# Optimization experiments

Measured on AMD Instinct MI355X. Metric: run time of the kernel, lower is better.

Reference implementation:

```python
import jax, jax.numpy as jnp
import numpy as np

N, IN_DIM, OUT_DIM, HEADS = 50000, 256, 256, 8
C = OUT_DIM // HEADS  # per-head channels = 32
E = 800000
G = 64  # number of graphs in the batch
NEG_SLOPE = 0.2
GN_EPS = 1e-5


def setup_inputs() -> dict:
    key = jax.random.key(0)
    ks = jax.random.split(key, 12)
    x = jax.random.normal(ks[0], (N, IN_DIM), dtype=jnp.float32)
    edge_index = jax.random.randint(ks[1], (2, E), 0, N, dtype=jnp.int64)
    batch = jnp.sort(jax.random.randint(ks[2], (N,), 0, G, dtype=jnp.int64))
    s = 1.0 / np.sqrt(IN_DIM)
    W_l = jax.random.uniform(ks[3], (IN_DIM, HEADS * C), jnp.float32, -s, s)
    b_l = jnp.zeros((HEADS * C,), jnp.float32)
    W_r = jax.random.uniform(ks[4], (IN_DIM, HEADS * C), jnp.float32, -s, s)
    b_r = jnp.zeros((HEADS * C,), jnp.float32)
    att = jax.random.normal(ks[5], (HEADS, C), dtype=jnp.float32) / np.sqrt(C)
    bias = jnp.zeros((HEADS * C,), jnp.float32)
    gn_weight = jnp.ones((OUT_DIM,), jnp.float32)
    gn_bias = jnp.zeros((OUT_DIM,), jnp.float32)
    gn_mean_scale = jnp.ones((OUT_DIM,), jnp.float32)
    return {"x": x, "edge_index": edge_index, "batch": batch,
            "W_l": W_l, "b_l": b_l, "W_r": W_r, "b_r": b_r,
            "att": att, "bias": bias, "gn_weight": gn_weight,
            "gn_bias": gn_bias, "gn_mean_scale": gn_mean_scale}


def _gat_block(x, src, dst, batch, W_l, b_l, W_r, b_r, att, bias,
               gn_weight, gn_bias, gn_mean_scale):
    n = x.shape[0]
    # GATv2Conv (add_self_loops=True, concat=True)
    loops = jnp.arange(n, dtype=src.dtype)
    src = jnp.concatenate([src, loops])
    dst = jnp.concatenate([dst, loops])
    xl = (x @ W_l + b_l).reshape(n, HEADS, C)  # source transform
    xr = (x @ W_r + b_r).reshape(n, HEADS, C)  # target transform
    e = jax.nn.leaky_relu(xl[src] + xr[dst], NEG_SLOPE)  # [E', H, C]
    logits = jnp.einsum('ehc,hc->eh', e, att)            # [E', H]
    # segment softmax over incoming edges of each destination node
    m = jax.ops.segment_max(logits, dst, num_segments=n)
    alpha = jnp.exp(logits - m[dst])
    denom = jax.ops.segment_sum(alpha, dst, num_segments=n)
    alpha = alpha / (denom[dst] + 1e-16)
    msg = xl[src] * alpha[:, :, None]                    # [E', H, C]
    h = jax.ops.segment_sum(msg, dst, num_segments=n).reshape(n, HEADS * C) + bias
    # identity residual (in_dim == out_dim) + ELU
    h = jax.nn.elu(h + x)
    # GraphNorm (post-norm)
    counts = jnp.maximum(jax.ops.segment_sum(jnp.ones((n,), h.dtype), batch,
                                             num_segments=G), 1.0)
    mean = jax.ops.segment_sum(h, batch, num_segments=G) / counts[:, None]
    out0 = h - gn_mean_scale * mean[batch]
    var = jax.ops.segment_sum(out0 * out0, batch, num_segments=G) / counts[:, None]
    return gn_weight * out0 / jnp.sqrt(var[batch] + GN_EPS) + gn_bias


def reference(x, edge_index, batch, W_l, b_l, W_r, b_r, att, bias,
              gn_weight, gn_bias, gn_mean_scale):
    return _gat_block(x, edge_index[0], edge_index[1], batch,
                      W_l, b_l, W_r, b_r, att, bias,
                      gn_weight, gn_bias, gn_mean_scale)
```

## Files before the change

### kernel.cpp

```cpp
#include <hip/hip_runtime.h>
#include <hip/hip_bf16.h>
#include <stdint.h>

#define N_NODES 50000
#define MPAD    50048
#define IN_DIM  256
#define EDGES   800000
#define EPRIME  (EDGES + N_NODES)
#define NGRAPH  64
#define GN_EPS  1e-5f
#define ECPAD   53248
#define SEG     52
#define SEG4    13

typedef __attribute__((ext_vector_type(8))) short short8;
typedef __attribute__((ext_vector_type(4))) float floatx4;
typedef __attribute__((ext_vector_type(2))) float float2v;

__device__ __forceinline__ unsigned short f2b(float f) {
    uint32_t u = __float_as_uint(f);
    u += 0x7fffu + ((u >> 16) & 1u);
    return (unsigned short)(u >> 16);
}
__device__ __forceinline__ float b2f(unsigned short u) {
    return __uint_as_float(((uint32_t)u) << 16);
}

__global__ __launch_bounds__(256) void k_prep_w(const float* __restrict__ Wl,
                                                const float* __restrict__ Wr,
                                                unsigned short* __restrict__ Wt) {
    int idx = blockIdx.x * 256 + threadIdx.x;
    int n = idx >> 8, k = idx & 255;
    float v = (n < 256) ? Wl[k * 256 + n] : Wr[k * 256 + (n - 256)];
    Wt[idx] = f2b(v);
}

__global__ __launch_bounds__(512) void k_gemm(const float* __restrict__ x,
                                              const unsigned short* __restrict__ Wt,
                                              const float* __restrict__ bl,
                                              const float* __restrict__ br,
                                              unsigned short* __restrict__ XL,
                                              unsigned short* __restrict__ XR) {
    __shared__ unsigned short As[64 * 256];
    int rbase = blockIdx.x * 64;
    int tid = threadIdx.x;

#pragma unroll
    for (int it = 0; it < 4; ++it) {
        int c = it * 512 + tid;
        int row = c >> 5, ch = c & 31;
        int gr = rbase + row;
        float4 f0, f1;
        if (gr < N_NODES) {
            const float4* src = (const float4*)(x + (size_t)gr * 256 + ch * 8);
            f0 = src[0]; f1 = src[1];
        } else {
            f0 = make_float4(0.f,0.f,0.f,0.f); f1 = f0;
        }
        short8 hv;
        hv[0] = (short)f2b(f0.x); hv[1] = (short)f2b(f0.y);
        hv[2] = (short)f2b(f0.z); hv[3] = (short)f2b(f0.w);
        hv[4] = (short)f2b(f1.x); hv[5] = (short)f2b(f1.y);
        hv[6] = (short)f2b(f1.z); hv[7] = (short)f2b(f1.w);
        *(short8*)(As + row * 256 + (ch ^ (row & 7)) * 8) = hv;
    }
    __syncthreads();

    int w = tid >> 6;
    int l = tid & 63;
    int m = l & 15, q = l >> 4;

    floatx4 acc[4][4];
#pragma unroll
    for (int rf = 0; rf < 4; ++rf)
#pragma unroll
        for (int cf = 0; cf < 4; ++cf)
            acc[rf][cf] = (floatx4){0.f, 0.f, 0.f, 0.f};

    const unsigned short* wbase = Wt + (size_t)(w * 64) * 256;

#pragma unroll
    for (int kk = 0; kk < 8; ++kk) {
        short8 a[4];
#pragma unroll
        for (int rf = 0; rf < 4; ++rf) {
            int row = rf * 16 + m;
            int ch = (kk * 4 + q) ^ (row & 7);
            a[rf] = *(const short8*)(As + row * 256 + ch * 8);
        }
#pragma unroll
        for (int cf = 0; cf < 4; ++cf) {
            short8 b = *(const short8*)(wbase + (size_t)(cf * 16 + m) * 256 + kk * 32 + q * 8);
#pragma unroll
            for (int rf = 0; rf < 4; ++rf)
                acc[rf][cf] = __builtin_amdgcn_mfma_f32_16x16x32_bf16(b, a[rf], acc[rf][cf], 0, 0, 0);
        }
    }

    unsigned short* obase = (w < 4) ? XL : XR;
    const float* bptr = (w < 4) ? bl : br;
    int cb = (w & 3) * 64;
#pragma unroll
    for (int cf = 0; cf < 4; ++cf) {
        int chb = cb + cf * 16 + q * 4;
        float4 bv = *(const float4*)(bptr + chb);
#pragma unroll
        for (int rf = 0; rf < 4; ++rf) {
            int node = rbase + rf * 16 + m;
            ushort4 o;
            o.x = f2b(acc[rf][cf][0] + bv.x);
            o.y = f2b(acc[rf][cf][1] + bv.y);
            o.z = f2b(acc[rf][cf][2] + bv.z);
            o.w = f2b(acc[rf][cf][3] + bv.w);
            *(ushort4*)(obase + (size_t)node * 256 + chb) = o;
        }
    }
}

__global__ __launch_bounds__(256) void k_hist(const int* __restrict__ ei,
                                              const int* __restrict__ batch,
                                              int* __restrict__ ecount,
                                              int* __restrict__ ncount) {
    __shared__ int hist[NGRAPH];
    if (threadIdx.x < NGRAPH) hist[threadIdx.x] = 0;
    __syncthreads();
    int e = blockIdx.x * 256 + threadIdx.x;
    if (e < EPRIME) {
        int d = (e < EDGES) ? ei[EDGES + e] : (e - EDGES);
        atomicAdd(&ecount[d], 1);
    }
    if (e < N_NODES) atomicAdd(&hist[batch[e]], 1);
    __syncthreads();
    if (threadIdx.x < NGRAPH && hist[threadIdx.x])
        atomicAdd(&ncount[threadIdx.x], hist[threadIdx.x]);
}

__global__ __launch_bounds__(1024) void k_scan(const int* __restrict__ ecount,
                                               int* __restrict__ estart,
                                               int* __restrict__ ecursor) {
    __shared__ int buf[1024];
    int t = threadIdx.x;
    int base = t * SEG;
    int4 v[SEG4];
    int sum = 0;
#pragma unroll
    for (int j = 0; j < SEG4; ++j) {
        v[j] = ((const int4*)(ecount + base))[j];
        sum += v[j].x + v[j].y + v[j].z + v[j].w;
    }
    buf[t] = sum;
    __syncthreads();
    for (int off = 1; off < 1024; off <<= 1) {
        int p = (t >= off) ? buf[t - off] : 0;
        __syncthreads();
        buf[t] += p;
        __syncthreads();
    }
    int run = buf[t] - sum;
#pragma unroll
    for (int j = 0; j < SEG4; ++j) {
        int4 o;
        o.x = run; run += v[j].x;
        o.y = run; run += v[j].y;
        o.z = run; run += v[j].z;
        o.w = run; run += v[j].w;
        ((int4*)(estart + base))[j]  = o;
        ((int4*)(ecursor + base))[j] = o;
    }
}

__global__ __launch_bounds__(256) void k_scatter(const int* __restrict__ ei,
                                                 int* __restrict__ ecursor,
                                                 int* __restrict__ sedge) {
    int e = blockIdx.x * 256 + threadIdx.x;
    if (e >= EPRIME) return;
    int s, d;
    if (e < EDGES) { s = ei[e]; d = ei[EDGES + e]; }
    else           { s = d = e - EDGES; }
    int pos = atomicAdd(&ecursor[d], 1);
    sedge[pos] = s;
}

__global__ __launch_bounds__(256) void k_msg(const unsigned short* __restrict__ XL,
                                             const unsigned short* __restrict__ XRb,
                                             const float* __restrict__ x,
                                             const float* __restrict__ att,
                                             const float* __restrict__ bias,
                                             const int* __restrict__ sedge,
                                             const int* __restrict__ estart,
                                             const int* __restrict__ ecount,
                                             float* __restrict__ out) {
    int d = (int)((blockIdx.x * 256 + threadIdx.x) >> 6);
    int l = threadIdx.x & 63;
    int lofs = l * 8;

    float4 xin  = ((const float4*)(x + (size_t)d * 256))[l];
    float4 bvv  = ((const float4*)bias)[l];
    float4 attv = ((const float4*)att)[l];
    float2v att01 = {attv.x, attv.y}, att23 = {attv.z, attv.w};

    uint2 xru = ((const uint2*)(XRb + (size_t)d * 256))[l];
    float2v xr01, xr23;
    xr01[0] = __uint_as_float(xru.x << 16);
    xr01[1] = __uint_as_float(xru.x & 0xffff0000u);
    xr23[0] = __uint_as_float(xru.y << 16);
    xr23[1] = __uint_as_float(xru.y & 0xffff0000u);

    int s0  = __builtin_amdgcn_readfirstlane(estart[d]);
    int cnt = __builtin_amdgcn_readfirstlane(ecount[d]);
    int c1m = cnt - 1;

    auto ldrow = [&](int src) -> uint2 {
        size_t off = ((size_t)(uint32_t)__builtin_amdgcn_readfirstlane(src)) << 9;
        return *(const uint2*)((const char*)XL + off + lofs);
    };

    float den0 = 0.f, den1 = 0.f, den2 = 0.f, den3 = 0.f;
    float2v A01 = {0.f,0.f}, A23 = {0.f,0.f};
    float2v B01 = {0.f,0.f}, B23 = {0.f,0.f};
    float2v C01 = {0.f,0.f}, C23 = {0.f,0.f};
    float2v D01 = {0.f,0.f}, D23 = {0.f,0.f};

    auto proc = [&](uint2 U, float& den, float2v& R01, float2v& R23) {
        float2v x01, x23;
        x01[0] = __uint_as_float(U.x << 16);
        x01[1] = __uint_as_float(U.x & 0xffff0000u);
        x23[0] = __uint_as_float(U.y << 16);
        x23[1] = __uint_as_float(U.y & 0xffff0000u);
        float2v e01 = x01 + xr01, e23 = x23 + xr23;
        float2v f01 = e01 * 0.2f, f23 = e23 * 0.2f;
        e01[0] = fmaxf(e01[0], f01[0]); e01[1] = fmaxf(e01[1], f01[1]);
        e23[0] = fmaxf(e23[0], f23[0]); e23[1] = fmaxf(e23[1], f23[1]);
        float2v pp2 = e01 * att01 + e23 * att23;
        float pp = pp2[0] + pp2[1];
        {
            int pi = __float_as_int(pp);
            pp += __int_as_float(__builtin_amdgcn_update_dpp(0, pi, 0xB1, 0xF, 0xF, true));
            pi = __float_as_int(pp);
            pp += __int_as_float(__builtin_amdgcn_update_dpp(0, pi, 0x4E, 0xF, 0xF, true));
            pp += __shfl_xor(pp, 4);
        }
        float al = __expf(fminf(pp, 80.f));
        den += al;
        float2v al2 = {al, al};
        R01 += al2 * x01;
        R23 += al2 * x23;
    };

    uint2 P0 = ldrow(sedge[s0]);
    uint2 P1 = ldrow(sedge[s0 + min(1, c1m)]);
    uint2 P2 = ldrow(sedge[s0 + min(2, c1m)]);
    uint2 P3 = ldrow(sedge[s0 + min(3, c1m)]);

    int nq = cnt >> 2;
    for (int qq = 0; qq < nq; ++qq) {
        uint2 Q0 = P0, Q1 = P1, Q2 = P2, Q3 = P3;
        int nb = (qq + 1) << 2;
        int i0 = min(nb,     c1m), i1 = min(nb + 1, c1m);
        int i2 = min(nb + 2, c1m), i3 = min(nb + 3, c1m);
        P0 = ldrow(sedge[s0 + i0]);
        P1 = ldrow(sedge[s0 + i1]);
        P2 = ldrow(sedge[s0 + i2]);
        P3 = ldrow(sedge[s0 + i3]);
        proc(Q0, den0, A01, A23);
        proc(Q1, den1, B01, B23);
        proc(Q2, den2, C01, C23);
        proc(Q3, den3, D01, D23);
    }
    int rem = cnt & 3;
    if (rem > 0) proc(P0, den0, A01, A23);
    if (rem > 1) proc(P1, den1, B01, B23);
    if (rem > 2) proc(P2, den2, C01, C23);

    float inv = 1.f / ((den0 + den1) + (den2 + den3) + 1e-16f);
    A01 = (A01 + B01) + (C01 + D01);
    A23 = (A23 + B23) + (C23 + D23);

    float h0 = A01[0] * inv + bvv.x + xin.x; h0 = (h0 > 0.f) ? h0 : (__expf(h0) - 1.f);
    float h1 = A01[1] * inv + bvv.y + xin.y; h1 = (h1 > 0.f) ? h1 : (__expf(h1) - 1.f);
    float h2 = A23[0] * inv + bvv.z + xin.z; h2 = (h2 > 0.f) ? h2 : (__expf(h2) - 1.f);
    float h3 = A23[1] * inv + bvv.w + xin.w; h3 = (h3 > 0.f) ? h3 : (__expf(h3) - 1.f);
    ((float4*)(out + (size_t)d * 256))[l] = make_float4(h0, h1, h2, h3);
}

#define GN_ROWS 128
__global__ __launch_bounds__(256) void k_gn_sum(const float* __restrict__ h,
                                                const int* __restrict__ batch,
                                                float* __restrict__ gsum,
                                                float* __restrict__ gsq) {
    __shared__ int bsh[GN_ROWS];
    int r0 = blockIdx.x * GN_ROWS;
    for (int j = threadIdx.x; j < GN_ROWS; j += 256) {
        int i = r0 + j;
        bsh[j] = (i < N_NODES) ? batch[i] : -1;
    }
    __syncthreads();
    int c = threadIdx.x;
    float s1 = 0.f, s2 = 0.f;
    int g = bsh[0];
    for (int j = 0; j < GN_ROWS; ++j) {
        int i = r0 + j;
        if (i >= N_NODES) break;
        int bg = bsh[j];
        if (bg != g) {
            atomicAdd(&gsum[g * 256 + c], s1);
            atomicAdd(&gsq[g * 256 + c], s2);
            s1 = 0.f; s2 = 0.f; g = bg;
        }
        float v = h[(size_t)i * 256 + c];
        s1 += v; s2 += v * v;
    }
    atomicAdd(&gsum[g * 256 + c], s1);
    atomicAdd(&gsq[g * 256 + c], s2);
}

__global__ __launch_bounds__(256) void k_final(float* __restrict__ out,
                                               const int* __restrict__ batch,
                                               const float* __restrict__ gsum,
                                               const float* __restrict__ gsq,
                                               const int* __restrict__ ncount,
                                               const float* __restrict__ gnw,
                                               const float* __restrict__ gnb,
                                               const float* __restrict__ gms) {
    int idx = blockIdx.x * 256 + threadIdx.x;
    int i = idx >> 6, l = idx & 63;
    if (i >= N_NODES) return;
    int g = batch[i];
    float inv = 1.f / fmaxf((float)ncount[g], 1.f);
    float4 hv = ((const float4*)(out + (size_t)i * 256))[l];
    float4 ms = ((const float4*)(gsum + g * 256))[l];
    float4 qs = ((const float4*)(gsq  + g * 256))[l];
    float4 wv = ((const float4*)gnw)[l];
    float4 bv = ((const float4*)gnb)[l];
    float4 sv = ((const float4*)gms)[l];
    float4 o;
    {
        float m = ms.x * inv, q = qs.x * inv;
        o.x = wv.x * (hv.x - sv.x * m) * rsqrtf(q - m * m * sv.x * (2.f - sv.x) + GN_EPS) + bv.x;
    }
    {
        float m = ms.y * inv, q = qs.y * inv;
        o.y = wv.y * (hv.y - sv.y * m) * rsqrtf(q - m * m * sv.y * (2.f - sv.y) + GN_EPS) + bv.y;
    }
    {
        float m = ms.z * inv, q = qs.z * inv;
        o.z = wv.z * (hv.z - sv.z * m) * rsqrtf(q - m * m * sv.z * (2.f - sv.z) + GN_EPS) + bv.z;
    }
    {
        float m = ms.w * inv, q = qs.w * inv;
        o.w = wv.w * (hv.w - sv.w * m) * rsqrtf(q - m * m * sv.w * (2.f - sv.w) + GN_EPS) + bv.w;
    }
    ((float4*)(out + (size_t)i * 256))[l] = o;
}

extern "C" void kernel_launch(void* const* d_in, const int* in_sizes, int n_in,
                              void* d_out, int out_size, void* d_ws, size_t ws_size,
                              hipStream_t stream) {
    const float* x    = (const float*)d_in[0];
    const int*   ei   = (const int*)d_in[1];
    const int*   batch= (const int*)d_in[2];
    const float* Wl   = (const float*)d_in[3];
    const float* bl   = (const float*)d_in[4];
    const float* Wr   = (const float*)d_in[5];
    const float* br   = (const float*)d_in[6];
    const float* att  = (const float*)d_in[7];
    const float* bias = (const float*)d_in[8];
    const float* gnw  = (const float*)d_in[9];
    const float* gnb  = (const float*)d_in[10];
    const float* gms  = (const float*)d_in[11];
    float* out = (float*)d_out;

    char* p = (char*)d_ws;
    auto alloc = [&](size_t bytes) -> char* {
        char* r = p;
        p += (bytes + 255) & ~(size_t)255;
        return r;
    };
    unsigned short* Wt  = (unsigned short*)alloc((size_t)512 * 256 * 2);
    unsigned short* XL  = (unsigned short*)alloc((size_t)MPAD * 256 * 2);
    unsigned short* XRb = (unsigned short*)alloc((size_t)MPAD * 256 * 2);
    int* estart         = (int*)alloc((size_t)ECPAD * 4);
    int* ecursor        = (int*)alloc((size_t)ECPAD * 4);
    int* sedge          = (int*)alloc((size_t)EPRIME * 4);
    int* ecount         = (int*)alloc((size_t)ECPAD * 4);
    int* ncount         = (int*)alloc((size_t)NGRAPH * 4);
    float* gsum         = (float*)alloc((size_t)2 * NGRAPH * 256 * 4);
    float* gsq          = gsum + NGRAPH * 256;
    size_t zbytes = (size_t)((char*)(gsum + 2 * NGRAPH * 256) - (char*)ecount);
    hipMemsetAsync(ecount, 0, zbytes, stream);

    k_prep_w<<<512, 256, 0, stream>>>(Wl, Wr, Wt);
    k_gemm<<<MPAD / 64, 512, 0, stream>>>(x, Wt, bl, br, XL, XRb);

    k_hist<<<(EPRIME + 255) / 256, 256, 0, stream>>>(ei, batch, ecount, ncount);
    k_scan<<<1, 1024, 0, stream>>>(ecount, estart, ecursor);
    k_scatter<<<(EPRIME + 255) / 256, 256, 0, stream>>>(ei, ecursor, sedge);

    k_msg<<<N_NODES / 4, 256, 0, stream>>>(XL, XRb, x, att, bias,
                                           sedge, estart, ecount, out);

    k_gn_sum<<<(N_NODES + GN_ROWS - 1) / GN_ROWS, 256, 0, stream>>>(out, batch, gsum, gsq);
    k_final<<<N_NODES * 64 / 256, 256, 0, stream>>>(out, batch, gsum, gsq,
                                                    ncount, gnw, gnb, gms);
}
```

Measured before the change: 404.9 us.

## Parallelize edge-offset scan, pad edge list, pack bf16 conversions, unroll GraphNorm sums

Replaces the single-block 1024-thread scan with a three-kernel multi-block scan (block sums, scan of block sums, per-block scan), so the prefix sum over node degrees runs across many CUs. Pads the sorted edge array with 16 zeroed entries, which lets the message kernel prefetch neighbours without clamping indices. Also uses packed bf16x2 conversion intrinsics in the GEMM, a ds_swizzle in place of a shuffle for the cross-lane reduction, and a 4-row unrolled fast path with smaller row tiles in the GraphNorm sum kernel. The extra kernel launches add fixed overhead, and the padded prefetch reads edges that belong to the next node, though their values are never accumulated.

```diff
diff --git a/kernel.cpp b/kernel.cpp
--- a/kernel.cpp
+++ b/kernel.cpp
@@ -10,20 +10,22 @@
 #define NGRAPH  64
 #define GN_EPS  1e-5f
 #define ECPAD   53248
-#define SEG     52
-#define SEG4    13
+#define NBLK    208
 
 typedef __attribute__((ext_vector_type(8))) short short8;
 typedef __attribute__((ext_vector_type(4))) float floatx4;
 typedef __attribute__((ext_vector_type(2))) float float2v;
+
+__device__ __forceinline__ uint32_t pk2bf(float a, float b) {
+    union { __hip_bfloat162 h; uint32_t u; } cv;
+    cv.h = __float22bfloat162_rn(make_float2(a, b));
+    return cv.u;
+}
 
 __device__ __forceinline__ unsigned short f2b(float f) {
     uint32_t u = __float_as_uint(f);
     u += 0x7fffu + ((u >> 16) & 1u);
     return (unsigned short)(u >> 16);
-}
-__device__ __forceinline__ float b2f(unsigned short u) {
-    return __uint_as_float(((uint32_t)u) << 16);
 }
 
 __global__ __launch_bounds__(256) void k_prep_w(const float* __restrict__ Wl,
@@ -57,12 +59,10 @@
         } else {
             f0 = make_float4(0.f,0.f,0.f,0.f); f1 = f0;
         }
-        short8 hv;
-        hv[0] = (short)f2b(f0.x); hv[1] = (short)f2b(f0.y);
-        hv[2] = (short)f2b(f0.z); hv[3] = (short)f2b(f0.w);
-        hv[4] = (short)f2b(f1.x); hv[5] = (short)f2b(f1.y);
-        hv[6] = (short)f2b(f1.z); hv[7] = (short)f2b(f1.w);
-        *(short8*)(As + row * 256 + (ch ^ (row & 7)) * 8) = hv;
+        uint32_t p0 = pk2bf(f0.x, f0.y), p1 = pk2bf(f0.z, f0.w);
+        uint32_t p2 = pk2bf(f1.x, f1.y), p3 = pk2bf(f1.z, f1.w);
+        uint4 hv = make_uint4(p0, p1, p2, p3);
+        *(uint4*)(As + row * 256 + (ch ^ (row & 7)) * 8) = hv;
     }
     __syncthreads();
 
@@ -107,12 +107,10 @@
 #pragma unroll
         for (int rf = 0; rf < 4; ++rf) {
             int node = rbase + rf * 16 + m;
-            ushort4 o;
-            o.x = f2b(acc[rf][cf][0] + bv.x);
-            o.y = f2b(acc[rf][cf][1] + bv.y);
-            o.z = f2b(acc[rf][cf][2] + bv.z);
-            o.w = f2b(acc[rf][cf][3] + bv.w);
-            *(ushort4*)(obase + (size_t)node * 256 + chb) = o;
+            uint2 o;
+            o.x = pk2bf(acc[rf][cf][0] + bv.x, acc[rf][cf][1] + bv.y);
+            o.y = pk2bf(acc[rf][cf][2] + bv.z, acc[rf][cf][3] + bv.w);
+            *(uint2*)(obase + (size_t)node * 256 + chb) = o;
         }
     }
 }
@@ -120,7 +118,8 @@
 __global__ __launch_bounds__(256) void k_hist(const int* __restrict__ ei,
                                               const int* __restrict__ batch,
                                               int* __restrict__ ecount,
-                                              int* __restrict__ ncount) {
+                                              int* __restrict__ ncount,
+                                              int* __restrict__ sedge) {
     __shared__ int hist[NGRAPH];
     if (threadIdx.x < NGRAPH) hist[threadIdx.x] = 0;
     __syncthreads();
@@ -130,43 +129,58 @@
         atomicAdd(&ecount[d], 1);
     }
     if (e < N_NODES) atomicAdd(&hist[batch[e]], 1);
+    if (blockIdx.x == 0 && threadIdx.x < 16) sedge[EPRIME + threadIdx.x] = 0;
     __syncthreads();
     if (threadIdx.x < NGRAPH && hist[threadIdx.x])
         atomicAdd(&ncount[threadIdx.x], hist[threadIdx.x]);
 }
 
-__global__ __launch_bounds__(1024) void k_scan(const int* __restrict__ ecount,
-                                               int* __restrict__ estart,
-                                               int* __restrict__ ecursor) {
-    __shared__ int buf[1024];
+__global__ __launch_bounds__(256) void k_scan1(const int* __restrict__ ecount,
+                                               int* __restrict__ bsum) {
+    __shared__ int red[256];
+    int v = ecount[blockIdx.x * 256 + threadIdx.x];
+    red[threadIdx.x] = v;
+    __syncthreads();
+    for (int off = 128; off > 0; off >>= 1) {
+        if (threadIdx.x < off) red[threadIdx.x] += red[threadIdx.x + off];
+        __syncthreads();
+    }
+    if (threadIdx.x == 0) bsum[blockIdx.x] = red[0];
+}
+
+__global__ __launch_bounds__(256) void k_scan2(int* __restrict__ bsum) {
+    __shared__ int buf[256];
     int t = threadIdx.x;
-    int base = t * SEG;
-    int4 v[SEG4];
-    int sum = 0;
-#pragma unroll
-    for (int j = 0; j < SEG4; ++j) {
-        v[j] = ((const int4*)(ecount + base))[j];
-        sum += v[j].x + v[j].y + v[j].z + v[j].w;
-    }
-    buf[t] = sum;
-    __syncthreads();
-    for (int off = 1; off < 1024; off <<= 1) {
+    int v = (t < NBLK) ? bsum[t] : 0;
+    buf[t] = v;
+    __syncthreads();
+    for (int off = 1; off < 256; off <<= 1) {
         int p = (t >= off) ? buf[t - off] : 0;
         __syncthreads();
         buf[t] += p;
         __syncthreads();
     }
-    int run = buf[t] - sum;
-#pragma unroll
-    for (int j = 0; j < SEG4; ++j) {
-        int4 o;
-        o.x = run; run += v[j].x;
-        o.y = run; run += v[j].y;
-        o.z = run; run += v[j].z;
-        o.w = run; run += v[j].w;
-        ((int4*)(estart + base))[j]  = o;
-        ((int4*)(ecursor + base))[j] = o;
-    }
+    if (t < NBLK) bsum[t] = buf[t] - v;
+}
+
+__global__ __launch_bounds__(256) void k_scan3(const int* __restrict__ ecount,
+                                               const int* __restrict__ bsum,
+                                               int* __restrict__ estart,
+                                               int* __restrict__ ecursor) {
+    __shared__ int buf[256];
+    int b = blockIdx.x, t = threadIdx.x;
+    int v = ecount[b * 256 + t];
+    buf[t] = v;
+    __syncthreads();
+    for (int off = 1; off < 256; off <<= 1) {
+        int p = (t >= off) ? buf[t - off] : 0;
+        __syncthreads();
+        buf[t] += p;
+        __syncthreads();
+    }
+    int e = bsum[b] + buf[t] - v;
+    estart[b * 256 + t]  = e;
+    ecursor[b * 256 + t] = e;
 }
 
 __global__ __launch_bounds__(256) void k_scatter(const int* __restrict__ ei,
@@ -208,7 +222,6 @@
 
     int s0  = __builtin_amdgcn_readfirstlane(estart[d]);
     int cnt = __builtin_amdgcn_readfirstlane(ecount[d]);
-    int c1m = cnt - 1;
 
     auto ldrow = [&](int src) -> uint2 {
         size_t off = ((size_t)(uint32_t)__builtin_amdgcn_readfirstlane(src)) << 9;
@@ -238,7 +251,7 @@
             pp += __int_as_float(__builtin_amdgcn_update_dpp(0, pi, 0xB1, 0xF, 0xF, true));
             pi = __float_as_int(pp);
             pp += __int_as_float(__builtin_amdgcn_update_dpp(0, pi, 0x4E, 0xF, 0xF, true));
-            pp += __shfl_xor(pp, 4);
+            pp += __int_as_float(__builtin_amdgcn_ds_swizzle(__float_as_int(pp), 0x101F));
         }
         float al = __expf(fminf(pp, 80.f));
         den += al;
@@ -248,20 +261,18 @@
     };
 
     uint2 P0 = ldrow(sedge[s0]);
-    uint2 P1 = ldrow(sedge[s0 + min(1, c1m)]);
-    uint2 P2 = ldrow(sedge[s0 + min(2, c1m)]);
-    uint2 P3 = ldrow(sedge[s0 + min(3, c1m)]);
+    uint2 P1 = ldrow(sedge[s0 + 1]);
+    uint2 P2 = ldrow(sedge[s0 + 2]);
+    uint2 P3 = ldrow(sedge[s0 + 3]);
 
     int nq = cnt >> 2;
     for (int qq = 0; qq < nq; ++qq) {
         uint2 Q0 = P0, Q1 = P1, Q2 = P2, Q3 = P3;
-        int nb = (qq + 1) << 2;
-        int i0 = min(nb,     c1m), i1 = min(nb + 1, c1m);
-        int i2 = min(nb + 2, c1m), i3 = min(nb + 3, c1m);
-        P0 = ldrow(sedge[s0 + i0]);
-        P1 = ldrow(sedge[s0 + i1]);
-        P2 = ldrow(sedge[s0 + i2]);
-        P3 = ldrow(sedge[s0 + i3]);
+        int nb = s0 + (qq + 1) * 4;
+        P0 = ldrow(sedge[nb]);
+        P1 = ldrow(sedge[nb + 1]);
+        P2 = ldrow(sedge[nb + 2]);
+        P3 = ldrow(sedge[nb + 3]);
         proc(Q0, den0, A01, A23);
         proc(Q1, den1, B01, B23);
         proc(Q2, den2, C01, C23);
@@ -283,32 +294,44 @@
     ((float4*)(out + (size_t)d * 256))[l] = make_float4(h0, h1, h2, h3);
 }
 
-#define GN_ROWS 128
+#define GN_ROWS 64
 __global__ __launch_bounds__(256) void k_gn_sum(const float* __restrict__ h,
                                                 const int* __restrict__ batch,
                                                 float* __restrict__ gsum,
                                                 float* __restrict__ gsq) {
     __shared__ int bsh[GN_ROWS];
     int r0 = blockIdx.x * GN_ROWS;
-    for (int j = threadIdx.x; j < GN_ROWS; j += 256) {
-        int i = r0 + j;
-        bsh[j] = (i < N_NODES) ? batch[i] : -1;
+    if (threadIdx.x < GN_ROWS) {
+        int i = r0 + threadIdx.x;
+        bsh[threadIdx.x] = (i < N_NODES) ? batch[i] : -1;
     }
     __syncthreads();
     int c = threadIdx.x;
     float s1 = 0.f, s2 = 0.f;
     int g = bsh[0];
-    for (int j = 0; j < GN_ROWS; ++j) {
+    for (int j = 0; j < GN_ROWS; j += 4) {
         int i = r0 + j;
         if (i >= N_NODES) break;
-        int bg = bsh[j];
-        if (bg != g) {
-            atomicAdd(&gsum[g * 256 + c], s1);
-            atomicAdd(&gsq[g * 256 + c], s2);
-            s1 = 0.f; s2 = 0.f; g = bg;
-        }
-        float v = h[(size_t)i * 256 + c];
-        s1 += v; s2 += v * v;
+        bool full = (i + 3 < N_NODES);
+        if (full && bsh[j] == g && bsh[j + 3] == g) {
+            const float* hp = h + (size_t)i * 256 + c;
+            float v0 = hp[0], v1 = hp[256], v2 = hp[512], v3 = hp[768];
+            s1 += (v0 + v1) + (v2 + v3);
+            s2 += (v0 * v0 + v1 * v1) + (v2 * v2 + v3 * v3);
+        } else {
+            for (int jj = j; jj < j + 4; ++jj) {
+                int ii = r0 + jj;
+                if (ii >= N_NODES) break;
+                int bg = bsh[jj];
+                if (bg != g) {
+                    atomicAdd(&gsum[g * 256 + c], s1);
+                    atomicAdd(&gsq[g * 256 + c], s2);
+                    s1 = 0.f; s2 = 0.f; g = bg;
+                }
+                float v = h[(size_t)ii * 256 + c];
+                s1 += v; s2 += v * v;
+            }
+        }
     }
     atomicAdd(&gsum[g * 256 + c], s1);
     atomicAdd(&gsq[g * 256 + c], s2);
@@ -381,7 +404,8 @@
     unsigned short* XRb = (unsigned short*)alloc((size_t)MPAD * 256 * 2);
     int* estart         = (int*)alloc((size_t)ECPAD * 4);
     int* ecursor        = (int*)alloc((size_t)ECPAD * 4);
-    int* sedge          = (int*)alloc((size_t)EPRIME * 4);
+    int* sedge          = (int*)alloc((size_t)(EPRIME + 16) * 4);
+    int* bsum           = (int*)alloc((size_t)256 * 4);
     int* ecount         = (int*)alloc((size_t)ECPAD * 4);
     int* ncount         = (int*)alloc((size_t)NGRAPH * 4);
     float* gsum         = (float*)alloc((size_t)2 * NGRAPH * 256 * 4);
@@ -392,8 +416,10 @@
     k_prep_w<<<512, 256, 0, stream>>>(Wl, Wr, Wt);
     k_gemm<<<MPAD / 64, 512, 0, stream>>>(x, Wt, bl, br, XL, XRb);
 
-    k_hist<<<(EPRIME + 255) / 256, 256, 0, stream>>>(ei, batch, ecount, ncount);
-    k_scan<<<1, 1024, 0, stream>>>(ecount, estart, ecursor);
+    k_hist<<<(EPRIME + 255) / 256, 256, 0, stream>>>(ei, batch, ecount, ncount, sedge);
+    k_scan1<<<NBLK, 256, 0, stream>>>(ecount, bsum);
+    k_scan2<<<1, 256, 0, stream>>>(bsum);
+    k_scan3<<<NBLK, 256, 0, stream>>>(ecount, bsum, estart, ecursor);
     k_scatter<<<(EPRIME + 255) / 256, 256, 0, stream>>>(ei, ecursor, sedge);
 
     k_msg<<<N_NODES / 4, 256, 0, stream>>>(XL, XRb, x, att, bias,
```

New measurement: 359.7 us. 1.13x faster.
